# Kernel tuning notes

Hardware: AMD Instinct MI355X
Metric: run time of the kernel (lower is better)

## Reference

```python
import jax, jax.numpy as jnp
import numpy as np
from jax import lax

HID = 64
GROUPS = 4
EPS = 1e-5


def group_norm(x, w, b):
    # x: [B, C, H, W], GROUPS groups
    B, C, H, W = x.shape
    xg = x.reshape(B, GROUPS, C // GROUPS, H, W)
    mu = xg.mean(axis=(2, 3, 4), keepdims=True)
    var = xg.var(axis=(2, 3, 4), keepdims=True)
    xn = ((xg - mu) * lax.rsqrt(var + EPS)).reshape(B, C, H, W)
    return xn * w[:, None, None] + b[:, None, None]


def cell_step(x_t, h, c, W, gw, gb):
    # x_t: [B, Cin, H, W]; h, c: [B, HID, H, W]; W: [4*HID, Cin+HID, k, k]
    inp = jnp.concatenate([x_t, h], axis=1)
    gates = lax.conv_general_dilated(inp, W, (1, 1), 'SAME',
                                     dimension_numbers=('NCHW', 'OIHW', 'NCHW'))
    gates = group_norm(gates, gw, gb)
    i, f, o, g = jnp.split(gates, 4, axis=1)
    i, f, o = jax.nn.sigmoid(i), jax.nn.sigmoid(f), jax.nn.sigmoid(o)
    g = jnp.tanh(g)
    c_next = f * c + i * g
    h_next = o * jnp.tanh(c_next)
    return h_next, c_next


def run_direction(xt, W, gw, gb, reverse):
    # xt: [T, B, C, H, W]
    T, B, C, H, Wd = xt.shape
    h0 = jnp.zeros((B, HID, H, Wd), xt.dtype)
    c0 = jnp.zeros_like(h0)

    def step(carry, x_t):
        h, c = carry
        h, c = cell_step(x_t, h, c, W, gw, gb)
        return (h, c), h

    _, hs = lax.scan(step, (h0, c0), xt, reverse=reverse)
    return hs  # [T, B, HID, H, W] in time order


def setup_inputs() -> dict:
    key = jax.random.key(0)
    ks = jax.random.split(key, 12)
    B, T, C, H, W = 4, 16, 64, 64, 64
    k = 3
    G4 = 4 * HID
    x = jax.random.normal(ks[0], (B, T, C, H, W), jnp.float32)
    Wf = jax.random.normal(ks[1], (G4, C + HID, k, k), jnp.float32) * 0.02
    gnf_w = 1.0 + 0.1 * jax.random.normal(ks[2], (G4,), jnp.float32)
    gnf_b = 0.1 * jax.random.normal(ks[3], (G4,), jnp.float32)
    Wb = jax.random.normal(ks[4], (G4, C + HID, k, k), jnp.float32) * 0.02
    gnb_w = 1.0 + 0.1 * jax.random.normal(ks[5], (G4,), jnp.float32)
    gnb_b = 0.1 * jax.random.normal(ks[6], (G4,), jnp.float32)
    Wfu = jax.random.normal(ks[7], (HID, 2 * HID, 1, 1), jnp.float32) * 0.05
    bn_w = 1.0 + 0.1 * jax.random.normal(ks[8], (HID,), jnp.float32)
    bn_b = 0.1 * jax.random.normal(ks[9], (HID,), jnp.float32)
    return {"x": x, "Wf": Wf, "gnf_w": gnf_w, "gnf_b": gnf_b,
            "Wb": Wb, "gnb_w": gnb_w, "gnb_b": gnb_b,
            "Wfu": Wfu, "bn_w": bn_w, "bn_b": bn_b}


def reference(x, Wf, gnf_w, gnf_b, Wb, gnb_w, gnb_b, Wfu, bn_w, bn_b):
    B, T, C, H, W = x.shape
    xt = jnp.transpose(x, (1, 0, 2, 3, 4))  # [T, B, C, H, W]
    hf = run_direction(xt, Wf, gnf_w, gnf_b, reverse=False)
    hb = run_direction(xt, Wb, gnb_w, gnb_b, reverse=True)
    combined = jnp.concatenate([hf, hb], axis=2)  # [T, B, 2*HID, H, W]
    comb = combined.reshape(T * B, 2 * HID, H, W)
    fused = lax.conv_general_dilated(comb, Wfu, (1, 1), 'SAME',
                                     dimension_numbers=('NCHW', 'OIHW', 'NCHW'))
    # BatchNorm2d (training-mode batch statistics), then ReLU
    mu = fused.mean(axis=(0, 2, 3), keepdims=True)
    var = fused.var(axis=(0, 2, 3), keepdims=True)
    fused = (fused - mu) * lax.rsqrt(var + EPS)
    fused = fused * bn_w[:, None, None] + bn_b[:, None, None]
    fused = jax.nn.relu(fused)
    out = fused.reshape(T, B, HID, H, W).transpose(1, 0, 2, 3, 4)
    return out
```

## Files before the change

### kernel.cpp

```cpp
#include <hip/hip_runtime.h>
#include <math.h>

#define PX 4096
#define EPS 1e-5f

typedef __attribute__((ext_vector_type(8))) __bf16 bf16x8;
typedef __attribute__((ext_vector_type(4))) float f32x4;

static __device__ __forceinline__ unsigned short f2b(float f) {
    unsigned int u = __float_as_uint(f);
    u += 0x7FFFu + ((u >> 16) & 1u);
    return (unsigned short)(u >> 16);
}
static __device__ __forceinline__ float b2f(unsigned short u) {
    return __uint_as_float((unsigned int)u << 16);
}
static __device__ __forceinline__ float rcpf(float x) {
    return __builtin_amdgcn_rcpf(x);
}


__global__ __launch_bounds__(256) void wconv2_kernel(
    const float* __restrict__ Wf, const float* __restrict__ Wb,
    unsigned short* __restrict__ W2s)
{
    int idx = blockIdx.x * 256 + threadIdx.x;
    if (idx >= 589824) return;
    int within = idx & 2047;
    int grp = idx >> 11;
    int oc = within >> 5;
    int slot = (within >> 3) & 3;
    int j = within & 7;
    int tap = grp % 9;
    int rest = grp / 9;
    int icblk = rest & 3;
    int ocblk = (rest >> 2) & 3;
    int dir = rest >> 4;
    int c = slot ^ ((oc >> 1) & 3);
    int ic = icblk * 32 + c * 8 + j;
    int OC = ocblk * 64 + oc;
    const float* __restrict__ W = dir ? Wb : Wf;
    W2s[idx] = f2b(W[((size_t)OC * 128 + ic) * 9 + tap]);
}

__global__ __launch_bounds__(256) void wfu_pack_kernel(
    const float* __restrict__ Wfu, unsigned short* __restrict__ wfrag)
{
    int idx = blockIdx.x * 256 + threadIdx.x;
    if (idx >= 8192) return;
    int j = idx & 7;
    int l = (idx >> 3) & 63;
    int icblk = (idx >> 9) & 3;
    int ocb = idx >> 11;
    int oc = ocb * 16 + (l & 15);
    int ic = icblk * 32 + (l >> 4) * 8 + j;
    wfrag[idx] = f2b(Wfu[oc * 128 + ic]);
}

__global__ __launch_bounds__(256) void xconv_kernel(
    const float* __restrict__ x, unsigned short* __restrict__ xb)
{
    int bt = blockIdx.x >> 6;
    int px0 = (blockIdx.x & 63) * 64;
    __shared__ unsigned short sh[64 * 72];
    int tid = threadIdx.x;
    {
        int px_l = tid & 63;
        int ic4 = tid >> 6;
        const float* __restrict__ src = x + (size_t)bt * 64 * PX + px0 + px_l;
#pragma unroll
        for (int k = 0; k < 16; ++k) {
            int ic = ic4 * 16 + k;
            sh[px_l * 72 + ic] = f2b(src[(size_t)ic * PX]);
        }
    }
    __syncthreads();
    {
        int px_w = tid >> 2;
        int ch = tid & 3;
        uint4 v0 = *reinterpret_cast<const uint4*>(&sh[px_w * 72 + ch * 16]);
        uint4 v1 = *reinterpret_cast<const uint4*>(&sh[px_w * 72 + ch * 16 + 8]);
        unsigned short* dst = xb + ((size_t)bt * PX + px0 + px_w) * 64 + ch * 16;
        *reinterpret_cast<uint4*>(dst) = v0;
        *reinterpret_cast<uint4*>(dst + 8) = v1;
    }
}

__global__ __launch_bounds__(256) void conv_mfma_kernel(
    const unsigned short* __restrict__ xb, const unsigned short* __restrict__ comb_t,
    const unsigned short* __restrict__ W2s,
    unsigned short* __restrict__ gatesb, float* __restrict__ gnstats, int s)
{
    const int dirb = blockIdx.y;
    const int dir = dirb >> 2, b = dirb & 3;
    const int ocblk = blockIdx.x >> 4;
    const int pxt = blockIdx.x & 15;
    const int py0 = (pxt >> 1) * 8;
    const int pxc0 = (pxt & 1) * 32;
    const int t = dir ? (15 - s) : s;
    const int prev_t = dir ? (t + 1) : (t - 1);

    __shared__ __align__(16) unsigned short Wl[9 * 64 * 32];
    __shared__ __align__(16) unsigned short in_s[340 * 32];
    __shared__ float red[8];

    const int tid = threadIdx.x;
    const int w = tid >> 6;
    const int l = tid & 63;
    const int l15 = l & 15;
    const int l4 = l >> 4;

    const unsigned short* __restrict__ xpx = xb + (size_t)(b * 16 + t) * PX * 64;
    const unsigned short* __restrict__ hpx = comb_t
        + (size_t)(prev_t * 4 + b) * PX * 128 + dir * 64;

    f32x4 acc[4][4];
#pragma unroll
    for (int i = 0; i < 4; ++i)
#pragma unroll
        for (int j = 0; j < 4; ++j)
            acc[i][j] = (f32x4){0.f, 0.f, 0.f, 0.f};

    for (int icblk = 0; icblk < 4; ++icblk) {
        __syncthreads();
        {
            const unsigned short* __restrict__ wsrc = W2s
                + ((size_t)((dir * 4 + ocblk) * 4 + icblk) * 9) * 2048;
#pragma unroll
            for (int it = 0; it < 9; ++it) {
                int e = tid + it * 256;
                *reinterpret_cast<uint4*>(&Wl[e * 8]) =
                    *reinterpret_cast<const uint4*>(wsrc + e * 8);
            }
        }
        {
            const bool useh = icblk >= 2;
            const unsigned short* __restrict__ srcpx = useh
                ? (hpx + (icblk - 2) * 32) : (xpx + icblk * 32);
            const int rec = useh ? 128 : 64;
            const bool zero = useh && (s == 0);
#pragma unroll
            for (int it = 0; it < 6; ++it) {
                int idx = tid + it * 256;
                if (idx < 1360) {
                    int c = idx & 3;
                    int pl = idx >> 2;
                    int row = (pl * 241) >> 13;
                    int col = pl - row * 34;
                    int gy = py0 - 1 + row;
                    int gx = pxc0 - 1 + col;
                    bool valid = ((unsigned)gy < 64u) && ((unsigned)gx < 64u) && !zero;
                    uint4 v = make_uint4(0u, 0u, 0u, 0u);
                    if (valid)
                        v = *reinterpret_cast<const uint4*>(
                            srcpx + (size_t)(gy * 64 + gx) * rec + c * 8);
                    int woff = pl * 32 + ((c ^ ((pl >> 1) & 3)) * 8);
                    *reinterpret_cast<uint4*>(&in_s[woff]) = v;
                }
            }
        }
        __syncthreads();

#pragma unroll
        for (int tap = 0; tap < 9; ++tap) {
            const int dy = tap / 3, dx = tap % 3;
            bf16x8 av[4], bv[4];
#pragma unroll
            for (int mi = 0; mi < 4; ++mi) {
                int oc = mi * 16 + l15;
                int aoff = tap * 2048 + oc * 32 + ((l4 ^ ((oc >> 1) & 3)) * 8);
                av[mi] = *reinterpret_cast<const bf16x8*>(&Wl[aoff]);
            }
#pragma unroll
            for (int ni = 0; ni < 4; ++ni) {
                int nr = ni >> 1, nc = ni & 1;
                int pl = (2 * w + nr + dy) * 34 + nc * 16 + l15 + dx;
                int boff = pl * 32 + ((l4 ^ ((pl >> 1) & 3)) * 8);
                bv[ni] = *reinterpret_cast<const bf16x8*>(&in_s[boff]);
            }
#pragma unroll
            for (int mi = 0; mi < 4; ++mi)
#pragma unroll
                for (int ni = 0; ni < 4; ++ni)
                    acc[mi][ni] = __builtin_amdgcn_mfma_f32_16x16x32_bf16(
                        av[mi], bv[ni], acc[mi][ni], 0, 0, 0);
        }
    }

    float s1 = 0.f, s2 = 0.f;
    unsigned short* __restrict__ gbase = gatesb
        + ((size_t)dirb * 256 + (size_t)ocblk * 64) * PX;
#pragma unroll
    for (int mi = 0; mi < 4; ++mi)
#pragma unroll
        for (int ni = 0; ni < 4; ++ni) {
            int nr = ni >> 1, nc = ni & 1;
            int px = (py0 + 2 * w + nr) * 64 + pxc0 + nc * 16 + l15;
#pragma unroll
            for (int j = 0; j < 4; ++j) {
                float v = acc[mi][ni][j];
                int oc = mi * 16 + l4 * 4 + j;
                gbase[(size_t)oc * PX + px] = f2b(v);
                s1 += v;
                s2 += v * v;
            }
        }
    for (int off = 32; off; off >>= 1) {
        s1 += __shfl_down(s1, off);
        s2 += __shfl_down(s2, off);
    }
    if (l == 0) { red[w * 2] = s1; red[w * 2 + 1] = s2; }
    __syncthreads();
    if (tid == 0) {
        float a = red[0] + red[2] + red[4] + red[6];
        float q = red[1] + red[3] + red[5] + red[7];
        float* slot = gnstats + (((size_t)(s * 2 + dir) * 4 + b) * 4 + ocblk) * 2;
        atomicAdd(slot, a);
        atomicAdd(slot + 1, q);
    }
}

__global__ __launch_bounds__(256) void point_kernel2(
    const unsigned short* __restrict__ gatesb, const float* __restrict__ gnstats,
    const float* __restrict__ gnf_w, const float* __restrict__ gnf_b,
    const float* __restrict__ gnb_w, const float* __restrict__ gnb_b,
    float* __restrict__ cbuf, unsigned short* __restrict__ comb_t, int s)
{
    int idx = blockIdx.x * 256 + threadIdx.x;
    int pxl = idx & 7;
    int o8 = (idx >> 3) & 7;
    int pxh = (idx >> 6) & 511;
    int dirb = idx >> 15;
    int px = pxh * 8 + pxl;
    int dir = dirb >> 2, b = dirb & 3;

    __shared__ float gwl[256], gbl[256], mrs[8];
    int tid = threadIdx.x;
    {
        const float* __restrict__ gw = dir ? gnb_w : gnf_w;
        const float* __restrict__ gb = dir ? gnb_b : gnf_b;
        gwl[tid] = gw[tid];
        gbl[tid] = gb[tid];
    }
    if (tid < 4) {
        const float* slot = gnstats + ((size_t)(s * 2 + dir) * 4 + b) * 8 + tid * 2;
        const float invN = 1.0f / 262144.0f;
        float mean = slot[0] * invN;
        float var = slot[1] * invN - mean * mean;
        mrs[tid * 2] = mean;
        mrs[tid * 2 + 1] = rsqrtf(var + EPS);
    }
    __syncthreads();

    const unsigned short* __restrict__ gbase = gatesb + (size_t)dirb * 256 * PX + px;
    size_t cbase = ((size_t)dirb * 64 + o8 * 8) * PX + px;
    float m0 = mrs[0], r0 = mrs[1], m1 = mrs[2], r1 = mrs[3];
    float m2 = mrs[4], r2 = mrs[5], m3 = mrs[6], r3 = mrs[7];

    unsigned int packed[4];
#pragma unroll
    for (int cc = 0; cc < 8; ++cc) {
        int ch = o8 * 8 + cc;
        float g0 = b2f(gbase[(size_t)(ch) * PX]);
        float g1 = b2f(gbase[(size_t)(64 + ch) * PX]);
        float g2 = b2f(gbase[(size_t)(128 + ch) * PX]);
        float g3 = b2f(gbase[(size_t)(192 + ch) * PX]);
        float v0 = (g0 - m0) * r0 * gwl[ch] + gbl[ch];
        float v1 = (g1 - m1) * r1 * gwl[64 + ch] + gbl[64 + ch];
        float v2 = (g2 - m2) * r2 * gwl[128 + ch] + gbl[128 + ch];
        float v3 = (g3 - m3) * r3 * gwl[192 + ch] + gbl[192 + ch];
        float ig = rcpf(1.f + __expf(-v0));
        float fg = rcpf(1.f + __expf(-v1));
        float og = rcpf(1.f + __expf(-v2));
        float gg = 1.f - 2.f * rcpf(1.f + __expf(2.f * v3));
        float cold = cbuf[cbase + (size_t)cc * PX];
        float cnew = fg * cold + ig * gg;
        float th = 1.f - 2.f * rcpf(1.f + __expf(2.f * cnew));
        float hnew = og * th;
        cbuf[cbase + (size_t)cc * PX] = cnew;
        unsigned int hb = (unsigned int)f2b(hnew);
        if (cc & 1) packed[cc >> 1] |= hb << 16;
        else        packed[cc >> 1] = hb;
    }
    int t = dir ? (15 - s) : s;
    size_t co = ((size_t)(t * 4 + b) * PX + px) * 128 + dir * 64 + o8 * 8;
    *reinterpret_cast<uint4*>(comb_t + co) =
        make_uint4(packed[0], packed[1], packed[2], packed[3]);
}

__global__ __launch_bounds__(256) void fuse_stats2_kernel(
    const unsigned short* __restrict__ comb_t,
    const unsigned short* __restrict__ wfrag, float* __restrict__ bnparts)
{
    int n = blockIdx.x >> 4, pxb = blockIdx.x & 15;
    int tid = threadIdx.x;
    int w = tid >> 6, l = tid & 63;
    int l15 = l & 15, l4 = l >> 4;

    bf16x8 B[4][4];
#pragma unroll
    for (int ocb = 0; ocb < 4; ++ocb)
#pragma unroll
        for (int icblk = 0; icblk < 4; ++icblk)
            B[ocb][icblk] = *reinterpret_cast<const bf16x8*>(
                wfrag + (((ocb * 4 + icblk) * 64 + l) * 8));

    f32x4 acc[4][4];
#pragma unroll
    for (int i = 0; i < 4; ++i)
#pragma unroll
        for (int j = 0; j < 4; ++j)
            acc[i][j] = (f32x4){0.f, 0.f, 0.f, 0.f};

    int px0 = pxb * 256 + w * 64;
    const unsigned short* __restrict__ cb = comb_t + (size_t)n * PX * 128;
#pragma unroll
    for (int ps = 0; ps < 4; ++ps) {
        const unsigned short* ab = cb + (size_t)(px0 + ps * 16 + l15) * 128 + l4 * 8;
        bf16x8 A[4];
#pragma unroll
        for (int icblk = 0; icblk < 4; ++icblk)
            A[icblk] = *reinterpret_cast<const bf16x8*>(ab + icblk * 32);
#pragma unroll
        for (int icblk = 0; icblk < 4; ++icblk)
#pragma unroll
            for (int ocb = 0; ocb < 4; ++ocb)
                acc[ps][ocb] = __builtin_amdgcn_mfma_f32_16x16x32_bf16(
                    A[icblk], B[ocb][icblk], acc[ps][ocb], 0, 0, 0);
    }

    float s1[4] = {0, 0, 0, 0}, s2[4] = {0, 0, 0, 0};
#pragma unroll
    for (int ps = 0; ps < 4; ++ps)
#pragma unroll
        for (int ocb = 0; ocb < 4; ++ocb)
#pragma unroll
            for (int j = 0; j < 4; ++j) {
                float v = acc[ps][ocb][j];
                s1[ocb] += v;
                s2[ocb] += v * v;
            }
#pragma unroll
    for (int ocb = 0; ocb < 4; ++ocb) {
        s1[ocb] += __shfl_down(s1[ocb], 32);
        s1[ocb] += __shfl_down(s1[ocb], 16);
        s2[ocb] += __shfl_down(s2[ocb], 32);
        s2[ocb] += __shfl_down(s2[ocb], 16);
    }
    __shared__ float sred[4][4][16][2];
    if (l < 16)
#pragma unroll
        for (int ocb = 0; ocb < 4; ++ocb) {
            sred[w][ocb][l][0] = s1[ocb];
            sred[w][ocb][l][1] = s2[ocb];
        }
    __syncthreads();
    if (tid < 128) {
        int oc = tid >> 1, isq = tid & 1;
        float v = sred[0][oc >> 4][oc & 15][isq] + sred[1][oc >> 4][oc & 15][isq]
                + sred[2][oc >> 4][oc & 15][isq] + sred[3][oc >> 4][oc & 15][isq];
        atomicAdd(bnparts + (blockIdx.x & 7) * 128 + tid, v);
    }
}

__global__ __launch_bounds__(256) void bn_apply2_kernel(
    const unsigned short* __restrict__ comb_t,
    const unsigned short* __restrict__ wfrag, const float* __restrict__ bnparts,
    const float* __restrict__ bn_w, const float* __restrict__ bn_b,
    float* __restrict__ out)
{
    int n = blockIdx.x >> 4, pxb = blockIdx.x & 15;
    int tid = threadIdx.x;
    int w = tid >> 6, l = tid & 63;
    int l15 = l & 15, l4 = l >> 4;

    __shared__ float sc[64], sh[64];
    if (tid < 64) {
        const float invN = 1.0f / 262144.0f;
        float S = 0.f, Q = 0.f;
#pragma unroll
        for (int p = 0; p < 8; ++p) {
            S += bnparts[p * 128 + tid * 2];
            Q += bnparts[p * 128 + tid * 2 + 1];
        }
        float mean = S * invN;
        float var = Q * invN - mean * mean;
        float scale = rsqrtf(var + EPS) * bn_w[tid];
        sc[tid] = scale;
        sh[tid] = bn_b[tid] - mean * scale;
    }

    bf16x8 B[4][4];
#pragma unroll
    for (int ocb = 0; ocb < 4; ++ocb)
#pragma unroll
        for (int icblk = 0; icblk < 4; ++icblk)
            B[ocb][icblk] = *reinterpret_cast<const bf16x8*>(
                wfrag + (((ocb * 4 + icblk) * 64 + l) * 8));
    __syncthreads();

    f32x4 acc[4][4];
#pragma unroll
    for (int i = 0; i < 4; ++i)
#pragma unroll
        for (int j = 0; j < 4; ++j)
            acc[i][j] = (f32x4){0.f, 0.f, 0.f, 0.f};

    int px0 = pxb * 256 + w * 64;
    const unsigned short* __restrict__ cb = comb_t + (size_t)n * PX * 128;
#pragma unroll
    for (int ps = 0; ps < 4; ++ps) {
        const unsigned short* ab = cb + (size_t)(px0 + ps * 16 + l15) * 128 + l4 * 8;
        bf16x8 A[4];
#pragma unroll
        for (int icblk = 0; icblk < 4; ++icblk)
            A[icblk] = *reinterpret_cast<const bf16x8*>(ab + icblk * 32);
#pragma unroll
        for (int icblk = 0; icblk < 4; ++icblk)
#pragma unroll
            for (int ocb = 0; ocb < 4; ++ocb)
                acc[ps][ocb] = __builtin_amdgcn_mfma_f32_16x16x32_bf16(
                    A[icblk], B[ocb][icblk], acc[ps][ocb], 0, 0, 0);
    }

    int t = n >> 2, bb = n & 3;
#pragma unroll
    for (int ps = 0; ps < 4; ++ps)
#pragma unroll
        for (int ocb = 0; ocb < 4; ++ocb) {
            int oc = ocb * 16 + l15;
            float scale = sc[oc], shift = sh[oc];
            float4 v;
            v.x = fmaxf(acc[ps][ocb][0] * scale + shift, 0.f);
            v.y = fmaxf(acc[ps][ocb][1] * scale + shift, 0.f);
            v.z = fmaxf(acc[ps][ocb][2] * scale + shift, 0.f);
            v.w = fmaxf(acc[ps][ocb][3] * scale + shift, 0.f);
            float* op = out + ((size_t)((bb * 16 + t) * 64 + oc)) * PX
                      + px0 + ps * 16 + l4 * 4;
            *reinterpret_cast<float4*>(op) = v;
        }
}

extern "C" void kernel_launch(void* const* d_in, const int* in_sizes, int n_in,
                              void* d_out, int out_size, void* d_ws, size_t ws_size,
                              hipStream_t stream) {
    const float* x     = (const float*)d_in[0];
    const float* Wf    = (const float*)d_in[1];
    const float* gnf_w = (const float*)d_in[2];
    const float* gnf_b = (const float*)d_in[3];
    const float* Wb    = (const float*)d_in[4];
    const float* gnb_w = (const float*)d_in[5];
    const float* gnb_b = (const float*)d_in[6];
    const float* Wfu   = (const float*)d_in[7];
    const float* bn_w  = (const float*)d_in[8];
    const float* bn_b  = (const float*)d_in[9];
    float* out = (float*)d_out;

    float* ws = (float*)d_ws;
    unsigned short* comb_t = (unsigned short*)ws;
    unsigned short* gatesb = (unsigned short*)(ws + 16777216);
    float* cbuf    = ws + 20971520;
    float* gnstats = ws + 23068672;
    float* bnparts = ws + 23069696;
    unsigned short* W2s   = (unsigned short*)(ws + 23070720);
    unsigned short* wfrag = (unsigned short*)(ws + 23365632);
    unsigned short* xb    = (unsigned short*)(ws + 23369728);

    hipMemsetAsync(cbuf, 0, (size_t)(2097152ll + 2048) * 4, stream);

    wconv2_kernel<<<2304, 256, 0, stream>>>(Wf, Wb, W2s);
    wfu_pack_kernel<<<32, 256, 0, stream>>>(Wfu, wfrag);
    xconv_kernel<<<4096, 256, 0, stream>>>(x, xb);

    for (int s = 0; s < 16; ++s) {
        conv_mfma_kernel<<<dim3(64, 8), 256, 0, stream>>>(
            xb, comb_t, W2s, gatesb, gnstats, s);
        point_kernel2<<<1024, 256, 0, stream>>>(
            gatesb, gnstats, gnf_w, gnf_b, gnb_w, gnb_b, cbuf, comb_t, s);
    }
    fuse_stats2_kernel<<<1024, 256, 0, stream>>>(comb_t, wfrag, bnparts);
    bn_apply2_kernel<<<1024, 256, 0, stream>>>(comb_t, wfrag, bnparts, bn_w, bn_b, out);
}
```

Baseline: 653.8 us.

## Load conv weights directly from global in MFMA fragment order and double-buffer input tiles

Repacks the conv weights into per-lane MFMA fragment order so each wave reads A operands straight from global/L2 instead of staging a 36KB weight tile in LDS. The freed LDS holds a double-buffered input halo tile, so the next channel block's loads are issued before the current block's MFMAs. One barrier per channel block is dropped, and the launch bound now requests higher occupancy. The cost is that weights are re-read from cache by every wave on every tap, which puts load latency on the MFMA critical path. The tighter register budget may also cause spills.

```diff
diff --git a/kernel.cpp b/kernel.cpp
--- a/kernel.cpp
+++ b/kernel.cpp
@@ -20,27 +20,25 @@
 }
 
 
-__global__ __launch_bounds__(256) void wconv2_kernel(
+__global__ __launch_bounds__(256) void wconv3_kernel(
     const float* __restrict__ Wf, const float* __restrict__ Wb,
-    unsigned short* __restrict__ W2s)
+    unsigned short* __restrict__ W3)
 {
     int idx = blockIdx.x * 256 + threadIdx.x;
     if (idx >= 589824) return;
-    int within = idx & 2047;
-    int grp = idx >> 11;
-    int oc = within >> 5;
-    int slot = (within >> 3) & 3;
-    int j = within & 7;
-    int tap = grp % 9;
-    int rest = grp / 9;
-    int icblk = rest & 3;
-    int ocblk = (rest >> 2) & 3;
-    int dir = rest >> 4;
-    int c = slot ^ ((oc >> 1) & 3);
-    int ic = icblk * 32 + c * 8 + j;
-    int OC = ocblk * 64 + oc;
+    int j = idx & 7;
+    int l = (idx >> 3) & 63;
+    int mi = (idx >> 9) & 3;
+    int g = idx >> 11;
+    int tap = g % 9;
+    int gg = g / 9;
+    int icblk = gg & 3;
+    int ocblk = (gg >> 2) & 3;
+    int dir = gg >> 4;
+    int oc = ocblk * 64 + mi * 16 + (l & 15);
+    int ic = icblk * 32 + (l >> 4) * 8 + j;
     const float* __restrict__ W = dir ? Wb : Wf;
-    W2s[idx] = f2b(W[((size_t)OC * 128 + ic) * 9 + tap]);
+    W3[idx] = f2b(W[((size_t)oc * 128 + ic) * 9 + tap]);
 }
 
 __global__ __launch_bounds__(256) void wfu_pack_kernel(
@@ -86,9 +84,9 @@
     }
 }
 
-__global__ __launch_bounds__(256) void conv_mfma_kernel(
+__global__ __launch_bounds__(256, 3) void conv_mfma_kernel(
     const unsigned short* __restrict__ xb, const unsigned short* __restrict__ comb_t,
-    const unsigned short* __restrict__ W2s,
+    const unsigned short* __restrict__ W3,
     unsigned short* __restrict__ gatesb, float* __restrict__ gnstats, int s)
 {
     const int dirb = blockIdx.y;
@@ -100,8 +98,7 @@
     const int t = dir ? (15 - s) : s;
     const int prev_t = dir ? (t + 1) : (t - 1);
 
-    __shared__ __align__(16) unsigned short Wl[9 * 64 * 32];
-    __shared__ __align__(16) unsigned short in_s[340 * 32];
+    __shared__ __align__(16) unsigned short in_s[2][340 * 32];
     __shared__ float red[8];
 
     const int tid = threadIdx.x;
@@ -121,62 +118,57 @@
         for (int j = 0; j < 4; ++j)
             acc[i][j] = (f32x4){0.f, 0.f, 0.f, 0.f};
 
+    auto stage = [&](int icblk, int buf) {
+        const bool useh = icblk >= 2;
+        const unsigned short* __restrict__ srcpx = useh
+            ? (hpx + (icblk - 2) * 32) : (xpx + icblk * 32);
+        const int rec = useh ? 128 : 64;
+        const bool zero = useh && (s == 0);
+#pragma unroll
+        for (int it = 0; it < 6; ++it) {
+            int idx = tid + it * 256;
+            if (idx < 1360) {
+                int c = idx & 3;
+                int pl = idx >> 2;
+                int row = (pl * 241) >> 13;
+                int col = pl - row * 34;
+                int gy = py0 - 1 + row;
+                int gx = pxc0 - 1 + col;
+                bool valid = ((unsigned)gy < 64u) && ((unsigned)gx < 64u) && !zero;
+                uint4 v = make_uint4(0u, 0u, 0u, 0u);
+                if (valid)
+                    v = *reinterpret_cast<const uint4*>(
+                        srcpx + (size_t)(gy * 64 + gx) * rec + c * 8);
+                int woff = pl * 32 + ((c ^ ((pl >> 1) & 3)) * 8);
+                *reinterpret_cast<uint4*>(&in_s[buf][woff]) = v;
+            }
+        }
+    };
+
+    stage(0, 0);
+
     for (int icblk = 0; icblk < 4; ++icblk) {
         __syncthreads();
-        {
-            const unsigned short* __restrict__ wsrc = W2s
-                + ((size_t)((dir * 4 + ocblk) * 4 + icblk) * 9) * 2048;
-#pragma unroll
-            for (int it = 0; it < 9; ++it) {
-                int e = tid + it * 256;
-                *reinterpret_cast<uint4*>(&Wl[e * 8]) =
-                    *reinterpret_cast<const uint4*>(wsrc + e * 8);
-            }
-        }
-        {
-            const bool useh = icblk >= 2;
-            const unsigned short* __restrict__ srcpx = useh
-                ? (hpx + (icblk - 2) * 32) : (xpx + icblk * 32);
-            const int rec = useh ? 128 : 64;
-            const bool zero = useh && (s == 0);
-#pragma unroll
-            for (int it = 0; it < 6; ++it) {
-                int idx = tid + it * 256;
-                if (idx < 1360) {
-                    int c = idx & 3;
-                    int pl = idx >> 2;
-                    int row = (pl * 241) >> 13;
-                    int col = pl - row * 34;
-                    int gy = py0 - 1 + row;
-                    int gx = pxc0 - 1 + col;
-                    bool valid = ((unsigned)gy < 64u) && ((unsigned)gx < 64u) && !zero;
-                    uint4 v = make_uint4(0u, 0u, 0u, 0u);
-                    if (valid)
-                        v = *reinterpret_cast<const uint4*>(
-                            srcpx + (size_t)(gy * 64 + gx) * rec + c * 8);
-                    int woff = pl * 32 + ((c ^ ((pl >> 1) & 3)) * 8);
-                    *reinterpret_cast<uint4*>(&in_s[woff]) = v;
-                }
-            }
-        }
-        __syncthreads();
+        if (icblk < 3) stage(icblk + 1, (icblk + 1) & 1);
+
+        const unsigned short* __restrict__ wb = W3
+            + ((size_t)((dir * 4 + ocblk) * 4 + icblk) * 9) * 2048;
+        const unsigned short* __restrict__ ib = in_s[icblk & 1];
 
 #pragma unroll
         for (int tap = 0; tap < 9; ++tap) {
             const int dy = tap / 3, dx = tap % 3;
             bf16x8 av[4], bv[4];
 #pragma unroll
-            for (int mi = 0; mi < 4; ++mi) {
-                int oc = mi * 16 + l15;
-                int aoff = tap * 2048 + oc * 32 + ((l4 ^ ((oc >> 1) & 3)) * 8);
-                av[mi] = *reinterpret_cast<const bf16x8*>(&Wl[aoff]);
-            }
+            for (int mi = 0; mi < 4; ++mi)
+                av[mi] = *reinterpret_cast<const bf16x8*>(
+                    wb + (tap * 4 + mi) * 512 + l * 8);
 #pragma unroll
             for (int ni = 0; ni < 4; ++ni) {
                 int nr = ni >> 1, nc = ni & 1;
                 int pl = (2 * w + nr + dy) * 34 + nc * 16 + l15 + dx;
                 int boff = pl * 32 + ((l4 ^ ((pl >> 1) & 3)) * 8);
-                bv[ni] = *reinterpret_cast<const bf16x8*>(&in_s[boff]);
+                bv[ni] = *reinterpret_cast<const bf16x8*>(&ib[boff]);
             }
 #pragma unroll
             for (int mi = 0; mi < 4; ++mi)
@@ -462,19 +454,19 @@
     float* cbuf    = ws + 20971520;
     float* gnstats = ws + 23068672;
     float* bnparts = ws + 23069696;
-    unsigned short* W2s   = (unsigned short*)(ws + 23070720);
+    unsigned short* W3    = (unsigned short*)(ws + 23070720);
     unsigned short* wfrag = (unsigned short*)(ws + 23365632);
     unsigned short* xb    = (unsigned short*)(ws + 23369728);
 
     hipMemsetAsync(cbuf, 0, (size_t)(2097152ll + 2048) * 4, stream);
 
-    wconv2_kernel<<<2304, 256, 0, stream>>>(Wf, Wb, W2s);
+    wconv3_kernel<<<2304, 256, 0, stream>>>(Wf, Wb, W3);
     wfu_pack_kernel<<<32, 256, 0, stream>>>(Wfu, wfrag);
     xconv_kernel<<<4096, 256, 0, stream>>>(x, xb);
 
     for (int s = 0; s < 16; ++s) {
         conv_mfma_kernel<<<dim3(64, 8), 256, 0, stream>>>(
-            xb, comb_t, W2s, gatesb, gnstats, s);
+            xb, comb_t, W3, gatesb, gnstats, s);
         point_kernel2<<<1024, 256, 0, stream>>>(
             gatesb, gnstats, gnf_w, gnf_b, gnb_w, gnb_b, cbuf, comb_t, s);
     }
```

Result: slower. 1.147 ms (+75.4%).
